# Optimization experiments

Hardware: AMD Instinct MI355X
Metric: run time of the kernel (lower is better)

## Reference

```python
import jax, jax.numpy as jnp
import numpy as np

N_EMBD = 1024
N_HEAD = 16
HEAD_SIZE = N_EMBD // N_HEAD


def setup_inputs() -> dict:
    key = jax.random.key(0)
    k_x, k_w, k_b = jax.random.split(key, 3)
    B, T, C = 2, 2048, N_EMBD
    x = jax.random.normal(k_x, (B, T, C), dtype=jnp.float32)
    # Linear(n_embd, 3*n_embd): weight [C, 3C] (applied as x @ W), bias [3C]
    w_qkv = jax.random.normal(k_w, (C, 3 * C), dtype=jnp.float32) * (1.0 / np.sqrt(C))
    b_qkv = jax.random.normal(k_b, (3 * C,), dtype=jnp.float32) * 0.02
    return {"x": x, "w_qkv": w_qkv, "b_qkv": b_qkv}


def reference(x, w_qkv, b_qkv):
    B, T, C = x.shape
    H, D = N_HEAD, HEAD_SIZE
    qkv = x @ w_qkv + b_qkv                      # [B, T, 3C]
    q, k, v = jnp.split(qkv, 3, axis=-1)         # each [B, T, C]
    # [B, T, C] -> [B, H, T, D]
    q = q.reshape(B, T, H, D).transpose(0, 2, 1, 3)
    k = k.reshape(B, T, H, D).transpose(0, 2, 1, 3)
    v = v.reshape(B, T, H, D).transpose(0, 2, 1, 3)
    scores = jnp.einsum('bhqd,bhkd->bhqk', q, k) / jnp.sqrt(jnp.float32(D))
    causal = jnp.tril(jnp.ones((T, T), dtype=bool))  # allow j <= i
    scores = jnp.where(causal[None, None, :, :], scores, -jnp.inf)
    weights = jax.nn.softmax(scores, axis=-1)    # [B, H, T, T]
    out = jnp.einsum('bhqk,bhkd->bhqd', weights, v)
    out = out.transpose(0, 2, 1, 3).reshape(B, T, C)
    return out
```

## Files before the change

### kernel.cpp

```cpp
#include <hip/hip_runtime.h>
#include <hip/hip_bf16.h>


#define CDIM  1024
#define C3    3072
#define HS    64
#define TLEN  2048
#define KVT   128
#define KSTR  72
#define VSTR  136
#define SCL   0.1803368801111204f

typedef __attribute__((ext_vector_type(8))) short bf16x8;
typedef __attribute__((ext_vector_type(4))) float f32x4;
typedef __attribute__((ext_vector_type(4))) unsigned short u16x4;

__device__ __forceinline__ unsigned short f2b(float f) {
    unsigned u = __float_as_uint(f);
    unsigned r = (u + 0x7FFFu + ((u >> 16) & 1u)) >> 16;
    return (unsigned short)r;
}
__device__ __forceinline__ float b2f(unsigned short u) {
    return __uint_as_float(((unsigned)u) << 16);
}
__device__ __forceinline__ float fexp2(float x) {
    return __builtin_amdgcn_exp2f(x);
}
__device__ __forceinline__ unsigned pkbf(float a, float b) {
    float2 f; f.x = a; f.y = b;
    __hip_bfloat162 h = __float22bfloat162_rn(f);
    union { __hip_bfloat162 h2; unsigned u; } c;
    c.h2 = h;
    return c.u;
}
__device__ __forceinline__ void gl_lds16(const unsigned short* g, unsigned short* l) {
    __builtin_amdgcn_global_load_lds((const __attribute__((address_space(1))) void*)g,
                                     (__attribute__((address_space(3))) void*)l, 16, 0, 0);
}
__device__ __forceinline__ int detect_bf(const void* bias, int lane) {
    unsigned w = ((const unsigned*)bias)[lane];
    unsigned e = (w >> 7) & 0xFF;
    unsigned long long m = __ballot(e >= 100 && e <= 135);
    return __popcll(m) >= 48;
}

__global__ __launch_bounds__(256) void k_prep(const void* __restrict__ w,
                                              const void* __restrict__ x,
                                              const void* __restrict__ bias,
                                              unsigned short* __restrict__ wt,
                                              unsigned short* __restrict__ xb) {
    __shared__ unsigned short tile[64 * 66];
    int t = threadIdx.x;
    int isbf = detect_bf(bias, t & 63);
    int bid = blockIdx.x;

    if (bid < 768) {
        int n0 = (bid % 48) * 64;
        int k0 = (bid / 48) * 64;
        for (int i = 0; i < 16; ++i) {
            int idx = t + i * 256;
            int r = idx >> 6, c = idx & 63;
            unsigned short v;
            if (isbf) v = ((const unsigned short*)w)[(k0 + r) * C3 + n0 + c];
            else      v = f2b(((const float*)w)[(k0 + r) * C3 + n0 + c]);
            tile[r * 66 + c] = v;
        }
        __syncthreads();
        for (int i = 0; i < 16; ++i) {
            int idx = t + i * 256;
            int r = idx >> 6, c = idx & 63;
            wt[(n0 + r) * CDIM + k0 + c] = tile[c * 66 + r];
        }
    }
    if (!isbf) {
        const float* s = (const float*)x;
        unsigned* d = (unsigned*)xb;
        int base = bid * 1024;
        for (int j = t; j < 1024; j += 256) {
            int idx = base + j;
            float a = s[2 * idx], b = s[2 * idx + 1];
            d[idx] = (unsigned)f2b(a) | ((unsigned)f2b(b) << 16);
        }
    }
}

__global__ __launch_bounds__(256, 3) void k_gemm_qkv(const void* __restrict__ xraw,
                                                     const unsigned short* __restrict__ xb,
                                                     const void* __restrict__ biasraw,
                                                     const unsigned short* __restrict__ Bt,
                                                     unsigned short* __restrict__ qk,
                                                     unsigned short* __restrict__ vtg) {
    __shared__ __align__(16) unsigned short As[128 * 64];
    __shared__ __align__(16) unsigned short Bs[128 * 64];
    int tid  = threadIdx.x;
    int lane = tid & 63, wv = tid >> 6;
    int quad = lane >> 4, l16 = lane & 15;
    int isbf = detect_bf(biasraw, lane);
    const unsigned short* A = isbf ? (const unsigned short*)xraw : xb;

    int m0 = blockIdx.y * 128, n0 = blockIdx.x * 128;
    int wm = (wv >> 1) * 64, wn = (wv & 1) * 64;

    f32x4 acc[4][4] = {};

    int srow = wv * 8 + (lane >> 3);
    int kcg8 = (((lane & 7) ^ (lane >> 3)) * 8);
    const unsigned short* Ag = A  + (m0 + srow) * CDIM + kcg8;
    const unsigned short* Bg = Bt + (n0 + srow) * CDIM + kcg8;
    unsigned short* lA = &As[srow * 64 + (lane & 7) * 8];
    unsigned short* lB = &Bs[srow * 64 + (lane & 7) * 8];

    for (int k0 = 0; k0 < CDIM; k0 += 64) {
        __syncthreads();
        for (int j = 0; j < 4; ++j) {
            gl_lds16(Ag + j * (32 * CDIM), lA + j * (32 * 64));
            gl_lds16(Bg + j * (32 * CDIM), lB + j * (32 * 64));
        }
        Ag += 64; Bg += 64;
        __syncthreads();

        for (int kk = 0; kk < 2; ++kk) {
            int sw = (l16 & 7);
            bf16x8 af[4], bfr[4];
            for (int mt = 0; mt < 4; ++mt)
                af[mt] = *(const bf16x8*)&As[(wm + mt * 16 + l16) * 64 + (((kk * 4 + quad) ^ sw) * 8)];
            for (int nt = 0; nt < 4; ++nt)
                bfr[nt] = *(const bf16x8*)&Bs[(wn + nt * 16 + l16) * 64 + (((kk * 4 + quad) ^ sw) * 8)];
            for (int mt = 0; mt < 4; ++mt)
                for (int nt = 0; nt < 4; ++nt)
                    acc[mt][nt] = __builtin_amdgcn_mfma_f32_16x16x32_bf16(af[mt], bfr[nt], acc[mt][nt], 0, 0, 0);
        }
    }

    if (n0 < 2048) {
        for (int mt = 0; mt < 4; ++mt) {
            int row = m0 + wm + mt * 16 + quad * 4;
            for (int nt = 0; nt < 4; ++nt) {
                int col = n0 + wn + nt * 16 + l16;
                float bv = isbf ? b2f(((const unsigned short*)biasraw)[col])
                                : ((const float*)biasraw)[col];
                for (int i = 0; i < 4; ++i)
                    qk[(row + i) * 2048 + col] = f2b(acc[mt][nt][i] + bv);
            }
        }
    } else {
        for (int mt = 0; mt < 4; ++mt) {
            int row = m0 + wm + mt * 16 + quad * 4;
            int t = row & 2047, b = row >> 11;
            for (int nt = 0; nt < 4; ++nt) {
                int col = n0 + wn + nt * 16 + l16;
                float bv = isbf ? b2f(((const unsigned short*)biasraw)[col])
                                : ((const float*)biasraw)[col];
                int hh = (col - 2048) >> 6, d = (col - 2048) & 63;
                u16x4 pk;
                for (int i = 0; i < 4; ++i) pk[i] = f2b(acc[mt][nt][i] + bv);
                *(u16x4*)&vtg[((b * 16 + hh) * 64 + d) * TLEN + t] = pk;
            }
        }
    }
}

__global__ __launch_bounds__(256, 2) void k_attn(const unsigned short* __restrict__ qk,
                                                 const unsigned short* __restrict__ vtg,
                                                 const void* __restrict__ biasraw,
                                                 void* __restrict__ outv) {
    __shared__ __align__(16) unsigned short Ks[128 * KSTR];
    __shared__ __align__(16) unsigned short Vt[80 * VSTR];
    __shared__ __align__(16) unsigned short Pt[4][16 * VSTR];

    int tid  = threadIdx.x;
    int lane = tid & 63, wv = tid >> 6;
    int quad = lane >> 4, l16 = lane & 15;
    int isbf = detect_bf(biasraw, lane);
    int bh = blockIdx.x;
    int a  = blockIdx.y;
    int b = bh >> 4, h = bh & 15;
    int rowbase = b * TLEN;
    unsigned short* Pw = Pt[wv];

    for (int idx = tid; idx < 16 * VSTR; idx += 256) {
        int r = idx / VSTR, c = idx - r * VSTR;
        Vt[64 * VSTR + idx] = (r == 0 && c < 128) ? (unsigned short)0x3F80 : (unsigned short)0;
    }

    int sr  = tid >> 3;
    int sc8 = (tid & 7) * 8;

    for (int s = 0; s < 2; ++s) {
        int qt    = (s == 0) ? (4 * a + wv) : (127 - 4 * a - wv);
        int q0w   = qt * 16;
        int trips = (((s == 0) ? (4 * a) : (127 - 4 * a)) >> 3) + 1;

        bf16x8 qf[2];
        for (int kh = 0; kh < 2; ++kh)
            qf[kh] = *(const bf16x8*)&qk[(rowbase + q0w + l16) * 2048 + h * HS + kh * 32 + quad * 8];

        f32x4 oacc[5] = {};

        for (int t = 0; t < trips; ++t) {
            int kv0 = t * KVT;
            const unsigned short* kg = qk  + (rowbase + kv0 + sr) * 2048 + CDIM + h * HS + sc8;
            const unsigned short* vg = vtg + (bh * 64 + sr) * TLEN + kv0 + sc8;
            uint4 kr0 = *(const uint4*)kg;
            uint4 kr1 = *(const uint4*)(kg + 32 * 2048);
            uint4 kr2 = *(const uint4*)(kg + 64 * 2048);
            uint4 kr3 = *(const uint4*)(kg + 96 * 2048);
            uint4 vr0 = *(const uint4*)vg;
            uint4 vr1 = *(const uint4*)(vg + 64);
            uint4 vr2 = *(const uint4*)(vg + 32 * TLEN);
            uint4 vr3 = *(const uint4*)(vg + 32 * TLEN + 64);
            __syncthreads();
            *(uint4*)&Ks[sr * KSTR + sc8]         = kr0;
            *(uint4*)&Ks[(sr + 32) * KSTR + sc8]  = kr1;
            *(uint4*)&Ks[(sr + 64) * KSTR + sc8]  = kr2;
            *(uint4*)&Ks[(sr + 96) * KSTR + sc8]  = kr3;
            *(uint4*)&Vt[sr * VSTR + sc8]         = vr0;
            *(uint4*)&Vt[sr * VSTR + sc8 + 64]    = vr1;
            *(uint4*)&Vt[(sr + 32) * VSTR + sc8]      = vr2;
            *(uint4*)&Vt[(sr + 32) * VSTR + sc8 + 64] = vr3;
            __syncthreads();

            f32x4 sc[8];
            for (int nt = 0; nt < 8; ++nt) {
                bf16x8 kf0 = *(const bf16x8*)&Ks[(nt * 16 + l16) * KSTR + quad * 8];
                bf16x8 kf1 = *(const bf16x8*)&Ks[(nt * 16 + l16) * KSTR + 32 + quad * 8];
                f32x4 z = {};
                z = __builtin_amdgcn_mfma_f32_16x16x32_bf16(kf0, qf[0], z, 0, 0, 0);
                z = __builtin_amdgcn_mfma_f32_16x16x32_bf16(kf1, qf[1], z, 0, 0, 0);
                sc[nt] = z;
            }

            bool dm = (t == trips - 1);
            int q = q0w + l16;
            for (int nt = 0; nt < 8; ++nt) {
                float p[4];
                for (int i = 0; i < 4; ++i) {
                    float arg = fminf(fmaf(sc[nt][i], SCL, -12.0f), 30.0f);
                    if (dm) {
                        int kv = kv0 + nt * 16 + quad * 4 + i;
                        if (kv > q) arg = -1e30f;
                    }
                    p[i] = fexp2(arg);
                }
                uint2 pk;
                pk.x = pkbf(p[0], p[1]);
                pk.y = pkbf(p[2], p[3]);
                *(uint2*)&Pw[l16 * VSTR + nt * 16 + quad * 4] = pk;
            }

            for (int kh = 0; kh < 4; ++kh) {
                bf16x8 bp = *(const bf16x8*)&Pw[l16 * VSTR + kh * 32 + quad * 8];
                for (int dt = 0; dt < 5; ++dt) {
                    bf16x8 av = *(const bf16x8*)&Vt[(dt * 16 + l16) * VSTR + kh * 32 + quad * 8];
                    oacc[dt] = __builtin_amdgcn_mfma_f32_16x16x32_bf16(av, bp, oacc[dt], 0, 0, 0);
                }
            }
        }

        float ls  = __shfl(oacc[4][0], l16);
        float inv = 1.0f / ls;
        int q = q0w + l16;
        if (isbf) {
            unsigned short* out = (unsigned short*)outv;
            for (int dt = 0; dt < 4; ++dt) {
                u16x4 ov;
                for (int i = 0; i < 4; ++i) ov[i] = f2b(oacc[dt][i] * inv);
                *(u16x4*)&out[(rowbase + q) * CDIM + h * HS + dt * 16 + quad * 4] = ov;
            }
        } else {
            float* out = (float*)outv;
            for (int dt = 0; dt < 4; ++dt) {
                float4 ov;
                ov.x = oacc[dt][0] * inv; ov.y = oacc[dt][1] * inv;
                ov.z = oacc[dt][2] * inv; ov.w = oacc[dt][3] * inv;
                *(float4*)&out[(rowbase + q) * CDIM + h * HS + dt * 16 + quad * 4] = ov;
            }
        }
    }
}

extern "C" void kernel_launch(void* const* d_in, const int* in_sizes, int n_in,
                              void* d_out, int out_size, void* d_ws, size_t ws_size,
                              hipStream_t stream) {
    const void* x    = d_in[0];
    const void* w    = d_in[1];
    const void* bias = d_in[2];

    char* ws = (char*)d_ws;
    unsigned short* xb  = (unsigned short*)ws;
    unsigned short* wt  = (unsigned short*)(ws + (8u  << 20));
    unsigned short* qk  = (unsigned short*)(ws + (16u << 20));
    unsigned short* vtg = (unsigned short*)(ws + (32u << 20));

    k_prep<<<2048, 256, 0, stream>>>(w, x, bias, wt, xb);
    k_gemm_qkv<<<dim3(24, 32), 256, 0, stream>>>(x, xb, bias, wt, qk, vtg);
    k_attn<<<dim3(32, 16), 256, 0, stream>>>(qk, vtg, bias, d_out);
}
```

Baseline: 158.3 us.

## Give each wave 32 query rows and compute softmax row sums in registers

The attention kernel now has each wave own 32 contiguous query rows (two 16-row MFMA tiles) instead of two separate 16-row tiles paired front and back. Each K/V tile staged in LDS therefore feeds twice as many score and PV MFMAs, which halves K/V global loads and block barriers per unit of work. The softmax denominator is now accumulated from the exponentials in registers and reduced with lane shuffles, replacing the extra ones-row in V and its fifth MFMA column. The trade-off is that the old front/back pairing that balanced causal work is gone, so per-block work now ranges from 1 to 16 KV trips, and register pressure rises with the doubled accumulators.

```diff
diff --git a/kernel.cpp b/kernel.cpp
--- a/kernel.cpp
+++ b/kernel.cpp
@@ -165,114 +165,124 @@
                                                  const void* __restrict__ biasraw,
                                                  void* __restrict__ outv) {
     __shared__ __align__(16) unsigned short Ks[128 * KSTR];
-    __shared__ __align__(16) unsigned short Vt[80 * VSTR];
-    __shared__ __align__(16) unsigned short Pt[4][16 * VSTR];
+    __shared__ __align__(16) unsigned short Vt[64 * VSTR];
+    __shared__ __align__(16) unsigned short Pt[4][32 * VSTR];
 
     int tid  = threadIdx.x;
     int lane = tid & 63, wv = tid >> 6;
     int quad = lane >> 4, l16 = lane & 15;
     int isbf = detect_bf(biasraw, lane);
     int bh = blockIdx.x;
-    int a  = blockIdx.y;
+    int y  = blockIdx.y;
+    int a  = (y < 8) ? y : (23 - y);
     int b = bh >> 4, h = bh & 15;
     int rowbase = b * TLEN;
     unsigned short* Pw = Pt[wv];
 
-    for (int idx = tid; idx < 16 * VSTR; idx += 256) {
-        int r = idx / VSTR, c = idx - r * VSTR;
-        Vt[64 * VSTR + idx] = (r == 0 && c < 128) ? (unsigned short)0x3F80 : (unsigned short)0;
-    }
+    int c     = 4 * a + wv;
+    int q0w   = c * 32;
+    int trips = a + 1;
+
+    bf16x8 qf[2][2];
+    for (int qt = 0; qt < 2; ++qt)
+        for (int kh = 0; kh < 2; ++kh)
+            qf[qt][kh] = *(const bf16x8*)&qk[(rowbase + q0w + qt * 16 + l16) * 2048 + h * HS + kh * 32 + quad * 8];
+
+    f32x4 oacc[2][4] = {};
+    float lsum[2] = {0.f, 0.f};
 
     int sr  = tid >> 3;
     int sc8 = (tid & 7) * 8;
 
-    for (int s = 0; s < 2; ++s) {
-        int qt    = (s == 0) ? (4 * a + wv) : (127 - 4 * a - wv);
-        int q0w   = qt * 16;
-        int trips = (((s == 0) ? (4 * a) : (127 - 4 * a)) >> 3) + 1;
-
-        bf16x8 qf[2];
-        for (int kh = 0; kh < 2; ++kh)
-            qf[kh] = *(const bf16x8*)&qk[(rowbase + q0w + l16) * 2048 + h * HS + kh * 32 + quad * 8];
-
-        f32x4 oacc[5] = {};
-
-        for (int t = 0; t < trips; ++t) {
-            int kv0 = t * KVT;
-            const unsigned short* kg = qk  + (rowbase + kv0 + sr) * 2048 + CDIM + h * HS + sc8;
-            const unsigned short* vg = vtg + (bh * 64 + sr) * TLEN + kv0 + sc8;
-            uint4 kr0 = *(const uint4*)kg;
-            uint4 kr1 = *(const uint4*)(kg + 32 * 2048);
-            uint4 kr2 = *(const uint4*)(kg + 64 * 2048);
-            uint4 kr3 = *(const uint4*)(kg + 96 * 2048);
-            uint4 vr0 = *(const uint4*)vg;
-            uint4 vr1 = *(const uint4*)(vg + 64);
-            uint4 vr2 = *(const uint4*)(vg + 32 * TLEN);
-            uint4 vr3 = *(const uint4*)(vg + 32 * TLEN + 64);
-            __syncthreads();
-            *(uint4*)&Ks[sr * KSTR + sc8]         = kr0;
-            *(uint4*)&Ks[(sr + 32) * KSTR + sc8]  = kr1;
-            *(uint4*)&Ks[(sr + 64) * KSTR + sc8]  = kr2;
-            *(uint4*)&Ks[(sr + 96) * KSTR + sc8]  = kr3;
-            *(uint4*)&Vt[sr * VSTR + sc8]         = vr0;
-            *(uint4*)&Vt[sr * VSTR + sc8 + 64]    = vr1;
-            *(uint4*)&Vt[(sr + 32) * VSTR + sc8]      = vr2;
-            *(uint4*)&Vt[(sr + 32) * VSTR + sc8 + 64] = vr3;
-            __syncthreads();
-
-            f32x4 sc[8];
-            for (int nt = 0; nt < 8; ++nt) {
-                bf16x8 kf0 = *(const bf16x8*)&Ks[(nt * 16 + l16) * KSTR + quad * 8];
-                bf16x8 kf1 = *(const bf16x8*)&Ks[(nt * 16 + l16) * KSTR + 32 + quad * 8];
-                f32x4 z = {};
-                z = __builtin_amdgcn_mfma_f32_16x16x32_bf16(kf0, qf[0], z, 0, 0, 0);
-                z = __builtin_amdgcn_mfma_f32_16x16x32_bf16(kf1, qf[1], z, 0, 0, 0);
-                sc[nt] = z;
-            }
-
-            bool dm = (t == trips - 1);
-            int q = q0w + l16;
+    for (int t = 0; t < trips; ++t) {
+        int kv0 = t * KVT;
+        const unsigned short* kg = qk  + (rowbase + kv0 + sr) * 2048 + CDIM + h * HS + sc8;
+        const unsigned short* vg = vtg + (bh * 64 + sr) * TLEN + kv0 + sc8;
+        uint4 kr0 = *(const uint4*)kg;
+        uint4 kr1 = *(const uint4*)(kg + 32 * 2048);
+        uint4 kr2 = *(const uint4*)(kg + 64 * 2048);
+        uint4 kr3 = *(const uint4*)(kg + 96 * 2048);
+        uint4 vr0 = *(const uint4*)vg;
+        uint4 vr1 = *(const uint4*)(vg + 64);
+        uint4 vr2 = *(const uint4*)(vg + 32 * TLEN);
+        uint4 vr3 = *(const uint4*)(vg + 32 * TLEN + 64);
+        __syncthreads();
+        *(uint4*)&Ks[sr * KSTR + sc8]        = kr0;
+        *(uint4*)&Ks[(sr + 32) * KSTR + sc8] = kr1;
+        *(uint4*)&Ks[(sr + 64) * KSTR + sc8] = kr2;
+        *(uint4*)&Ks[(sr + 96) * KSTR + sc8] = kr3;
+        *(uint4*)&Vt[sr * VSTR + sc8]        = vr0;
+        *(uint4*)&Vt[sr * VSTR + sc8 + 64]   = vr1;
+        *(uint4*)&Vt[(sr + 32) * VSTR + sc8]      = vr2;
+        *(uint4*)&Vt[(sr + 32) * VSTR + sc8 + 64] = vr3;
+        __syncthreads();
+
+        f32x4 s0[8], s1[8];
+        for (int nt = 0; nt < 8; ++nt) {
+            bf16x8 kf0 = *(const bf16x8*)&Ks[(nt * 16 + l16) * KSTR + quad * 8];
+            bf16x8 kf1 = *(const bf16x8*)&Ks[(nt * 16 + l16) * KSTR + 32 + quad * 8];
+            f32x4 z0 = {}, z1 = {};
+            z0 = __builtin_amdgcn_mfma_f32_16x16x32_bf16(kf0, qf[0][0], z0, 0, 0, 0);
+            z0 = __builtin_amdgcn_mfma_f32_16x16x32_bf16(kf1, qf[0][1], z0, 0, 0, 0);
+            z1 = __builtin_amdgcn_mfma_f32_16x16x32_bf16(kf0, qf[1][0], z1, 0, 0, 0);
+            z1 = __builtin_amdgcn_mfma_f32_16x16x32_bf16(kf1, qf[1][1], z1, 0, 0, 0);
+            s0[nt] = z0; s1[nt] = z1;
+        }
+
+        bool dm = (t == trips - 1);
+        for (int qt = 0; qt < 2; ++qt) {
+            const f32x4* sv = qt ? s1 : s0;
+            int q = q0w + qt * 16 + l16;
+            float psum = 0.f;
             for (int nt = 0; nt < 8; ++nt) {
                 float p[4];
                 for (int i = 0; i < 4; ++i) {
-                    float arg = fminf(fmaf(sc[nt][i], SCL, -12.0f), 30.0f);
+                    float arg = fminf(fmaf(sv[nt][i], SCL, -12.0f), 30.0f);
                     if (dm) {
                         int kv = kv0 + nt * 16 + quad * 4 + i;
                         if (kv > q) arg = -1e30f;
                     }
                     p[i] = fexp2(arg);
+                    psum += p[i];
                 }
                 uint2 pk;
                 pk.x = pkbf(p[0], p[1]);
                 pk.y = pkbf(p[2], p[3]);
-                *(uint2*)&Pw[l16 * VSTR + nt * 16 + quad * 4] = pk;
-            }
-
-            for (int kh = 0; kh < 4; ++kh) {
-                bf16x8 bp = *(const bf16x8*)&Pw[l16 * VSTR + kh * 32 + quad * 8];
-                for (int dt = 0; dt < 5; ++dt) {
-                    bf16x8 av = *(const bf16x8*)&Vt[(dt * 16 + l16) * VSTR + kh * 32 + quad * 8];
-                    oacc[dt] = __builtin_amdgcn_mfma_f32_16x16x32_bf16(av, bp, oacc[dt], 0, 0, 0);
-                }
-            }
-        }
-
-        float ls  = __shfl(oacc[4][0], l16);
-        float inv = 1.0f / ls;
-        int q = q0w + l16;
+                *(uint2*)&Pw[(qt * 16 + l16) * VSTR + nt * 16 + quad * 4] = pk;
+            }
+            lsum[qt] += psum;
+        }
+
+        for (int kh = 0; kh < 4; ++kh) {
+            bf16x8 bp0 = *(const bf16x8*)&Pw[l16 * VSTR + kh * 32 + quad * 8];
+            bf16x8 bp1 = *(const bf16x8*)&Pw[(16 + l16) * VSTR + kh * 32 + quad * 8];
+            for (int dt = 0; dt < 4; ++dt) {
+                bf16x8 av = *(const bf16x8*)&Vt[(dt * 16 + l16) * VSTR + kh * 32 + quad * 8];
+                oacc[0][dt] = __builtin_amdgcn_mfma_f32_16x16x32_bf16(av, bp0, oacc[0][dt], 0, 0, 0);
+                oacc[1][dt] = __builtin_amdgcn_mfma_f32_16x16x32_bf16(av, bp1, oacc[1][dt], 0, 0, 0);
+            }
+        }
+    }
+
+    for (int qt = 0; qt < 2; ++qt) {
+        float l = lsum[qt];
+        l += __shfl_xor(l, 16);
+        l += __shfl_xor(l, 32);
+        float inv = 1.0f / l;
+        int q = q0w + qt * 16 + l16;
         if (isbf) {
             unsigned short* out = (unsigned short*)outv;
             for (int dt = 0; dt < 4; ++dt) {
                 u16x4 ov;
-                for (int i = 0; i < 4; ++i) ov[i] = f2b(oacc[dt][i] * inv);
+                for (int i = 0; i < 4; ++i) ov[i] = f2b(oacc[qt][dt][i] * inv);
                 *(u16x4*)&out[(rowbase + q) * CDIM + h * HS + dt * 16 + quad * 4] = ov;
             }
         } else {
             float* out = (float*)outv;
             for (int dt = 0; dt < 4; ++dt) {
                 float4 ov;
-                ov.x = oacc[dt][0] * inv; ov.y = oacc[dt][1] * inv;
-                ov.z = oacc[dt][2] * inv; ov.w = oacc[dt][3] * inv;
+                ov.x = oacc[qt][dt][0] * inv; ov.y = oacc[qt][dt][1] * inv;
+                ov.z = oacc[qt][dt][2] * inv; ov.w = oacc[qt][dt][3] * inv;
                 *(float4*)&out[(rowbase + q) * CDIM + h * HS + dt * 16 + quad * 4] = ov;
             }
         }
```

Result: slower. 166.1 us (+4.9%).
